# Optimization experiments

Hardware: AMD Instinct MI355X
Metric: run time of the kernel (lower is better)

## Reference

```python
import jax, jax.numpy as jnp
import numpy as np

LOG_STD_MAX = 2.0
LOG_STD_MIN = -5.0
N_LAYERS = 10
HID = 512
OBS = 21
ACT = 8
OVERALL = HID * (N_LAYERS + 1)          # 5632
IN_DIM = OBS + OVERALL                   # 5653
OUT_DIM = OVERALL + ACT                  # 5640
BATCH = 8192


def _block_banded_weight(rng):
    # staircase partitions, exactly as layer_init
    in_d = [0, OBS] + [OBS + HID * i for i in range(1, N_LAYERS + 2)]
    out_d = [0] + [HID * i for i in range(1, N_LAYERS + 2)] + [OUT_DIM]
    W = np.zeros((OUT_DIM, IN_DIM), dtype=np.float32)
    for i in range(N_LAYERS + 2):
        r0, r1 = out_d[i], out_d[i + 1]
        c0, c1 = in_d[i], in_d[i + 1]
        fan_in = c1 - c0
        std = np.sqrt(2.0 / fan_in)  # kaiming_normal_ fan_in, gain sqrt(2)
        W[r0:r1, c0:c1] = rng.standard_normal((r1 - r0, c1 - c0)).astype(np.float32) * std
    return jnp.asarray(W)


def setup_inputs() -> dict:
    key = jax.random.key(0)
    k1, k2, k3, k4, k5, k6 = jax.random.split(key, 6)
    rng = np.random.default_rng(0)
    return {
        "obs": jax.random.normal(k1, (BATCH, OBS), dtype=jnp.float32),
        "hidden0": jax.random.uniform(k2, (BATCH, OVERALL), dtype=jnp.float32),
        "prev_mean": jax.random.normal(k3, (BATCH, ACT), dtype=jnp.float32),
        "prev_logstd": jax.random.normal(k4, (BATCH, ACT), dtype=jnp.float32),
        "W_mean": _block_banded_weight(rng),
        "b_mean": jnp.zeros((OUT_DIM,), dtype=jnp.float32),
        "W_logstd": jax.random.normal(k5, (ACT, IN_DIM), dtype=jnp.float32) / np.sqrt(IN_DIM),
        "b_logstd": jax.random.normal(k6, (ACT,), dtype=jnp.float32) * 0.01,
    }


def reference(obs, hidden0, prev_mean, prev_logstd, W_mean, b_mean, W_logstd, b_logstd):
    x = jnp.concatenate([obs, hidden0], axis=1)            # [B, IN_DIM]
    new_x = x @ W_mean.T + b_mean                          # [B, OUT_DIM]
    new_hidden = jax.nn.relu(new_x[:, :-ACT])              # [B, OVERALL]
    new_mean = new_x[:, -ACT:]                             # [B, ACT]
    new_log_std = x @ W_logstd.T + b_logstd                # [B, ACT]
    # outputs come from the PREVIOUS step's (mean, log_std)
    log_std = jnp.tanh(prev_logstd)
    log_std = LOG_STD_MIN + 0.5 * (LOG_STD_MAX - LOG_STD_MIN) * (log_std + 1.0)
    return (prev_mean, log_std, new_hidden, new_mean, new_log_std)
```

## Files before the change

kernel.cpp:

```cpp
#include <hip/hip_runtime.h>
#include <math.h>

typedef unsigned short u16;
typedef unsigned int u32;
typedef __attribute__((ext_vector_type(8))) short short8;
typedef __attribute__((ext_vector_type(4))) float float4v;

#define BATCH   8192
#define OBS     21
#define HID     512
#define NL      10
#define OVERALL 5632
#define IN_DIM  5653
#define OUT_DIM 5640
#define ACT     8

#define O_PM   0
#define O_LS   65536
#define O_NH   131072
#define O_NM   (131072 + BATCH*OVERALL)
#define O_NLS  (O_NM + 65536)

#define WSP_TOTAL (10*512*512)
#define WSP_BYTES ((size_t)WSP_TOTAL * 2)

__device__ __forceinline__ u16 f2bf(float f) {
    u32 u = __float_as_uint(f);
    u32 r = (u + 0x7fffu + ((u >> 16) & 1u)) >> 16;
    return (u16)r;
}
__device__ __forceinline__ u32 pkbf(float a, float b) {
    return (u32)f2bf(a) | ((u32)f2bf(b) << 16);
}
__device__ __forceinline__ void gload_lds16(const void* g, void* l) {
    __builtin_amdgcn_global_load_lds(
        (const __attribute__((address_space(1))) char*)g,
        (__attribute__((address_space(3))) char*)l, 16, 0, 0);
}

__global__ __launch_bounds__(256) void k_pack(const float* __restrict__ Wm,
                                              u16* __restrict__ ws) {
    int idx = blockIdx.x * 256 + threadIdx.x;
    if (idx >= WSP_TOTAL) return;
    int z = idx >> 18;
    int rem = idx & 262143;
    int n = rem >> 9, k = rem & 511;
    float v = Wm[(size_t)(512 * (z + 1) + n) * IN_DIM + OBS + 512 * z + k];
    ws[idx] = f2bf(v);
}

#define BM 128
#define BN 128
#define BK 32
#define A_LD 40
__global__ __launch_bounds__(256, 2) void k_gemm(const float* __restrict__ X,
                                                 const float* __restrict__ Wm_raw,
                                                 const u16* __restrict__ Wp,
                                                 const float* __restrict__ b_mean,
                                                 float* __restrict__ out_h,
                                                 int packed) {
    __shared__ __attribute__((aligned(16))) u16 As[BM * A_LD];
    __shared__ __attribute__((aligned(16))) u16 Bs[BN * BK];
    int t = threadIdx.x;
    int wave = t >> 6, lane = t & 63;
    int quad = lane >> 4, r16 = lane & 15;
    int gm = blockIdx.x * BM;
    int gn = blockIdx.y * BN;
    int z = blockIdx.z;
    int wm = (wave >> 1) * 64;
    int wn = (wave & 1) * 64;
    int ar = t >> 1;
    int ah = t & 1;

    const float* Arow = X + (size_t)(gm + ar) * OVERALL + z * 512 + ah * 16;

    float4v acc[4][4];
#pragma unroll
    for (int i = 0; i < 4; i++)
#pragma unroll
        for (int j = 0; j < 4; j++) acc[i][j] = (float4v)0.f;

    for (int k0 = 0; k0 < 512; k0 += BK) {
        __syncthreads();
        {
            const float* ga = Arow + k0;
            float4 v0 = *(const float4*)(ga);
            float4 v1 = *(const float4*)(ga + 4);
            float4 v2 = *(const float4*)(ga + 8);
            float4 v3 = *(const float4*)(ga + 12);
            uint4 p0, p1;
            p0.x = pkbf(v0.x, v0.y); p0.y = pkbf(v0.z, v0.w);
            p0.z = pkbf(v1.x, v1.y); p0.w = pkbf(v1.z, v1.w);
            p1.x = pkbf(v2.x, v2.y); p1.y = pkbf(v2.z, v2.w);
            p1.z = pkbf(v3.x, v3.y); p1.w = pkbf(v3.z, v3.w);
            *(uint4*)&As[ar * A_LD + ah * 16] = p0;
            *(uint4*)&As[ar * A_LD + ah * 16 + 8] = p1;
        }
        if (packed) {
#pragma unroll
            for (int it = 0; it < 2; ++it) {
                int n = it * 64 + wave * 16 + (lane >> 2);
                int kk = (lane & 3) * 8;
                const u16* gb = Wp + (size_t)z * (512 * 512) + (size_t)(gn + n) * 512 + k0 + kk;
                gload_lds16(gb, (char*)Bs + it * 4096 + wave * 1024);
            }
        } else {
            int n = t >> 1, h = t & 1;
            const float* gb = Wm_raw + (size_t)(512 * (z + 1) + gn + n) * IN_DIM
                              + OBS + 512 * z + k0 + h * 16;
#pragma unroll
            for (int e = 0; e < 16; e += 2)
                *(u32*)&Bs[n * BK + h * 16 + e] = pkbf(gb[e], gb[e + 1]);
        }
        __syncthreads();

        short8 af[4], bf[4];
#pragma unroll
        for (int i = 0; i < 4; i++) {
            af[i] = *(const short8*)&As[(wm + i * 16 + r16) * A_LD + quad * 8];
            bf[i] = *(const short8*)&Bs[(wn + i * 16 + r16) * BK + quad * 8];
        }
#pragma unroll
        for (int i = 0; i < 4; i++)
#pragma unroll
            for (int j = 0; j < 4; j++)
                acc[i][j] = __builtin_amdgcn_mfma_f32_16x16x32_bf16(af[i], bf[j], acc[i][j], 0, 0, 0);
    }

    int colblock = 512 * (z + 1);
#pragma unroll
    for (int j = 0; j < 4; j++) {
        int n_loc = gn + wn + j * 16 + r16;
        float bias = b_mean[colblock + n_loc];
#pragma unroll
        for (int i = 0; i < 4; i++) {
            int m0 = gm + wm + i * 16 + quad * 4;
#pragma unroll
            for (int r = 0; r < 4; r++) {
                float v = acc[i][j][r] + bias;
                out_h[(size_t)(m0 + r) * OVERALL + colblock + n_loc] = fmaxf(v, 0.f);
            }
        }
    }
}

__global__ __launch_bounds__(256) void k_block0(const float* __restrict__ obs,
                                                const float* __restrict__ Wm,
                                                const float* __restrict__ b_mean,
                                                float* __restrict__ out_h) {
    __shared__ float obs_s[8 * OBS];
    int t = threadIdx.x;
    int b0 = blockIdx.x * 8;
    if (t < 8 * OBS) obs_s[t] = obs[(size_t)b0 * OBS + t];
    __syncthreads();
#pragma unroll
    for (int half = 0; half < 2; ++half) {
        int n = half * 256 + t;
        float w[OBS];
#pragma unroll
        for (int k = 0; k < OBS; k++) w[k] = Wm[(size_t)n * IN_DIM + k];
        float bias = b_mean[n];
#pragma unroll 2
        for (int r = 0; r < 8; r++) {
            float a = bias;
#pragma unroll
            for (int k = 0; k < OBS; k++) a += obs_s[r * OBS + k] * w[k];
            out_h[(size_t)(b0 + r) * OVERALL + n] = fmaxf(a, 0.f);
        }
    }
}

__global__ __launch_bounds__(256) void k_thin(const float* __restrict__ obs,
                                              const float* __restrict__ X,
                                              const float* __restrict__ Wm,
                                              const float* __restrict__ Wls,
                                              const float* __restrict__ b_mean,
                                              const float* __restrict__ b_logstd,
                                              float* __restrict__ out_mean,
                                              float* __restrict__ out_ls) {
    int t = threadIdx.x, wave = t >> 6, lane = t & 63;
    int b0 = (blockIdx.x * 4 + wave) * 4;

    float als[4][8], amn[4][8];
#pragma unroll
    for (int r = 0; r < 4; r++)
#pragma unroll
        for (int n = 0; n < 8; n++) { als[r][n] = 0.f; amn[r][n] = 0.f; }

    for (int j = 0; j < 22; j++) {
        int k = j * 256 + lane * 4;
        float x[4][4];
#pragma unroll
        for (int r = 0; r < 4; r++)
            *(float4*)x[r] = *(const float4*)(X + (size_t)(b0 + r) * OVERALL + k);
#pragma unroll
        for (int n = 0; n < 8; n++) {
            const float* wp = Wls + (size_t)n * IN_DIM + OBS + k;
            float w0 = wp[0], w1 = wp[1], w2 = wp[2], w3 = wp[3];
#pragma unroll
            for (int r = 0; r < 4; r++) {
                als[r][n] += x[r][0] * w0 + x[r][1] * w1 + x[r][2] * w2 + x[r][3] * w3;
            }
        }
        if (j >= 20) {
#pragma unroll
            for (int n = 0; n < 8; n++) {
                const float* wp = Wm + (size_t)(OVERALL + n) * IN_DIM + OBS + k;
                float w0 = wp[0], w1 = wp[1], w2 = wp[2], w3 = wp[3];
#pragma unroll
                for (int r = 0; r < 4; r++) {
                    amn[r][n] += x[r][0] * w0 + x[r][1] * w1 + x[r][2] * w2 + x[r][3] * w3;
                }
            }
        }
    }
    if (lane < OBS) {
#pragma unroll
        for (int r = 0; r < 4; r++) {
            float xo = obs[(size_t)(b0 + r) * OBS + lane];
#pragma unroll
            for (int n = 0; n < 8; n++)
                als[r][n] += xo * Wls[(size_t)n * IN_DIM + lane];
        }
    }
#pragma unroll
    for (int s = 1; s < 64; s <<= 1) {
#pragma unroll
        for (int r = 0; r < 4; r++)
#pragma unroll
            for (int n = 0; n < 8; n++) {
                als[r][n] += __shfl_xor(als[r][n], s, 64);
                amn[r][n] += __shfl_xor(amn[r][n], s, 64);
            }
    }
    if (lane == 0) {
#pragma unroll
        for (int r = 0; r < 4; r++)
#pragma unroll
            for (int n = 0; n < 8; n++) {
                out_ls[(size_t)(b0 + r) * ACT + n] = als[r][n] + b_logstd[n];
                out_mean[(size_t)(b0 + r) * ACT + n] = amn[r][n] + b_mean[OVERALL + n];
            }
    }
}

__global__ __launch_bounds__(256) void k_small(const float* __restrict__ pm,
                                               const float* __restrict__ pls,
                                               float* __restrict__ o0,
                                               float* __restrict__ o1) {
    int i = blockIdx.x * 256 + threadIdx.x;
    float4 a = *(const float4*)(pm + (size_t)i * 4);
    *(float4*)(o0 + (size_t)i * 4) = a;
    float4 b = *(const float4*)(pls + (size_t)i * 4);
    float4 o;
    o.x = -5.f + 3.5f * (tanhf(b.x) + 1.f);
    o.y = -5.f + 3.5f * (tanhf(b.y) + 1.f);
    o.z = -5.f + 3.5f * (tanhf(b.z) + 1.f);
    o.w = -5.f + 3.5f * (tanhf(b.w) + 1.f);
    *(float4*)(o1 + (size_t)i * 4) = o;
}

extern "C" void kernel_launch(void* const* d_in, const int* in_sizes, int n_in,
                              void* d_out, int out_size, void* d_ws, size_t ws_size,
                              hipStream_t stream) {
    const float* obs         = (const float*)d_in[0];
    const float* hidden0     = (const float*)d_in[1];
    const float* prev_mean   = (const float*)d_in[2];
    const float* prev_logstd = (const float*)d_in[3];
    const float* W_mean      = (const float*)d_in[4];
    const float* b_mean      = (const float*)d_in[5];
    const float* W_logstd    = (const float*)d_in[6];
    const float* b_logstd    = (const float*)d_in[7];

    float* out   = (float*)d_out;
    float* o_pm  = out + O_PM;
    float* o_ls  = out + O_LS;
    float* o_nh  = out + O_NH;
    float* o_nm  = out + O_NM;
    float* o_nls = out + O_NLS;
    u16*   ws    = (u16*)d_ws;

    int packed = (ws != nullptr && ws_size >= WSP_BYTES) ? 1 : 0;

    if (packed) {
        k_pack<<<(WSP_TOTAL + 255) / 256, 256, 0, stream>>>(W_mean, ws);
    }
    k_gemm<<<dim3(BATCH / BM, 512 / BN, NL), 256, 0, stream>>>(
        hidden0, W_mean, ws, b_mean, o_nh, packed);
    k_block0<<<BATCH / 8, 256, 0, stream>>>(obs, W_mean, b_mean, o_nh);
    k_thin<<<BATCH / 16, 256, 0, stream>>>(obs, hidden0, W_mean, W_logstd,
                                           b_mean, b_logstd, o_nm, o_nls);
    k_small<<<64, 256, 0, stream>>>(prev_mean, prev_logstd, o_pm, o_ls);
}
```

Baseline: 512.5 us.

## Fuse thin logstd/mean projections into block GEMM with full-width N tiles

Replaces the separate thin fp32 reduction kernel by computing the logstd and final-mean projections with bf16 MFMA inside the block-diagonal GEMM, each block reusing the activation tile already staged in LDS. Logstd partials are accumulated across z-slices with atomics into a pre-zeroed buffer. The GEMM now uses 1024-thread blocks covering all 512 output columns, with a swizzled B layout in LDS and register prefetch of the next A tile, so each activation tile is read once per slice instead of four times. The obs-block kernel caches its weights in LDS, and the small elementwise work merges into a finish kernel. The trade-offs are atomics, bf16 rounding on the logstd path, and a large LDS footprint per block.

Measured after the change: 452.3 us. 1.13x faster.

```diff
diff --git a/kernel.cpp b/kernel.cpp
--- a/kernel.cpp
+++ b/kernel.cpp
@@ -12,7 +12,6 @@
 #define NL      10
 #define OVERALL 5632
 #define IN_DIM  5653
-#define OUT_DIM 5640
 #define ACT     8
 
 #define O_PM   0
@@ -50,214 +49,242 @@
 }
 
 #define BM 128
-#define BN 128
 #define BK 32
-#define A_LD 40
-__global__ __launch_bounds__(256, 2) void k_gemm(const float* __restrict__ X,
-                                                 const float* __restrict__ Wm_raw,
-                                                 const u16* __restrict__ Wp,
-                                                 const float* __restrict__ b_mean,
-                                                 float* __restrict__ out_h,
-                                                 int packed) {
-    __shared__ __attribute__((aligned(16))) u16 As[BM * A_LD];
-    __shared__ __attribute__((aligned(16))) u16 Bs[BN * BK];
+#define LDA 40
+__global__ __launch_bounds__(1024, 4) void k_fused(
+        const float* __restrict__ X,
+        const float* __restrict__ Wm_raw,
+        const u16* __restrict__ Wp,
+        const float* __restrict__ Wls_raw,
+        const float* __restrict__ b_mean,
+        float* __restrict__ out_h,
+        float* __restrict__ out_ls,
+        float* __restrict__ out_mean,
+        int packed) {
+    __shared__ __attribute__((aligned(16))) u16 As[BM * LDA];
+    __shared__ __attribute__((aligned(16))) u16 Bs[512 * 32];
+    __shared__ __attribute__((aligned(16))) u16 Wt[16 * 520];
+    u16* Wt2 = (u16*)Bs;
+
     int t = threadIdx.x;
-    int wave = t >> 6, lane = t & 63;
+    int w = t >> 6, lane = t & 63;
     int quad = lane >> 4, r16 = lane & 15;
     int gm = blockIdx.x * BM;
-    int gn = blockIdx.y * BN;
-    int z = blockIdx.z;
-    int wm = (wave >> 1) * 64;
-    int wn = (wave & 1) * 64;
-    int ar = t >> 1;
-    int ah = t & 1;
-
-    const float* Arow = X + (size_t)(gm + ar) * OVERALL + z * 512 + ah * 16;
+    int z = blockIdx.y;
+    bool mainz = (z < 10);
+    int wm = (w >> 3) * 64;
+    int wn = (w & 7) * 64;
+
+    {
+        int n = t >> 7;
+        int k4 = (t & 127) * 4;
+        const float* wr = Wls_raw + (size_t)n * IN_DIM + OBS + z * 512 + k4;
+        u16* dst = &Wt[n * 520 + k4];
+        dst[0] = f2bf(wr[0]); dst[1] = f2bf(wr[1]);
+        dst[2] = f2bf(wr[2]); dst[3] = f2bf(wr[3]);
+        if (!mainz) {
+            const float* wr2 = Wm_raw + (size_t)(OVERALL + n) * IN_DIM + OBS + z * 512 + k4;
+            u16* d2 = &Wt2[n * 520 + k4];
+            d2[0] = f2bf(wr2[0]); d2[1] = f2bf(wr2[1]);
+            d2[2] = f2bf(wr2[2]); d2[3] = f2bf(wr2[3]);
+        }
+    }
+
+    int arow = t >> 3;
+    int acol = (t & 7) * 4;
+    const float* gA = X + (size_t)(gm + arow) * OVERALL + (size_t)z * 512 + acol;
+    float4 areg = *(const float4*)(gA);
 
     float4v acc[4][4];
 #pragma unroll
     for (int i = 0; i < 4; i++)
 #pragma unroll
         for (int j = 0; j < 4; j++) acc[i][j] = (float4v)0.f;
-
-    for (int k0 = 0; k0 < 512; k0 += BK) {
+    float4v accL = (float4v)0.f;
+
+    for (int it = 0; it < 16; ++it) {
+        int k0 = it * BK;
         __syncthreads();
         {
-            const float* ga = Arow + k0;
-            float4 v0 = *(const float4*)(ga);
-            float4 v1 = *(const float4*)(ga + 4);
-            float4 v2 = *(const float4*)(ga + 8);
-            float4 v3 = *(const float4*)(ga + 12);
-            uint4 p0, p1;
-            p0.x = pkbf(v0.x, v0.y); p0.y = pkbf(v0.z, v0.w);
-            p0.z = pkbf(v1.x, v1.y); p0.w = pkbf(v1.z, v1.w);
-            p1.x = pkbf(v2.x, v2.y); p1.y = pkbf(v2.z, v2.w);
-            p1.z = pkbf(v3.x, v3.y); p1.w = pkbf(v3.z, v3.w);
-            *(uint4*)&As[ar * A_LD + ah * 16] = p0;
-            *(uint4*)&As[ar * A_LD + ah * 16 + 8] = p1;
-        }
-        if (packed) {
-#pragma unroll
-            for (int it = 0; it < 2; ++it) {
-                int n = it * 64 + wave * 16 + (lane >> 2);
-                int kk = (lane & 3) * 8;
-                const u16* gb = Wp + (size_t)z * (512 * 512) + (size_t)(gn + n) * 512 + k0 + kk;
-                gload_lds16(gb, (char*)Bs + it * 4096 + wave * 1024);
-            }
-        } else {
-            int n = t >> 1, h = t & 1;
-            const float* gb = Wm_raw + (size_t)(512 * (z + 1) + gn + n) * IN_DIM
-                              + OBS + 512 * z + k0 + h * 16;
-#pragma unroll
-            for (int e = 0; e < 16; e += 2)
-                *(u32*)&Bs[n * BK + h * 16 + e] = pkbf(gb[e], gb[e + 1]);
+            uint2 p;
+            p.x = pkbf(areg.x, areg.y);
+            p.y = pkbf(areg.z, areg.w);
+            *(uint2*)&As[arow * LDA + acol] = p;
+        }
+        if (mainz) {
+            if (packed) {
+#pragma unroll
+                for (int i2 = 0; i2 < 2; ++i2) {
+                    int base_row = i2 * 256 + w * 16;
+                    int row = base_row + (lane >> 2);
+                    int slot = lane & 3;
+                    int j = (slot - row) & 3;
+                    const u16* g = Wp + (size_t)z * 262144 + (size_t)row * 512 + k0 + j * 8;
+                    gload_lds16(g, (char*)Bs + base_row * 64);
+                }
+            } else {
+#pragma unroll
+                for (int i2 = 0; i2 < 2; ++i2) {
+                    int row = i2 * 256 + w * 16 + (lane >> 2);
+                    int slot = lane & 3;
+                    int j = (slot - row) & 3;
+                    const float* g = Wm_raw + (size_t)(512 * (z + 1) + row) * IN_DIM
+                                     + OBS + (size_t)z * 512 + k0 + j * 8;
+                    uint4 q;
+                    q.x = pkbf(g[0], g[1]); q.y = pkbf(g[2], g[3]);
+                    q.z = pkbf(g[4], g[5]); q.w = pkbf(g[6], g[7]);
+                    *(uint4*)&Bs[row * 32 + slot * 8] = q;
+                }
+            }
         }
         __syncthreads();
-
-        short8 af[4], bf[4];
-#pragma unroll
-        for (int i = 0; i < 4; i++) {
-            af[i] = *(const short8*)&As[(wm + i * 16 + r16) * A_LD + quad * 8];
-            bf[i] = *(const short8*)&Bs[(wn + i * 16 + r16) * BK + quad * 8];
-        }
-#pragma unroll
-        for (int i = 0; i < 4; i++)
-#pragma unroll
-            for (int j = 0; j < 4; j++)
-                acc[i][j] = __builtin_amdgcn_mfma_f32_16x16x32_bf16(af[i], bf[j], acc[i][j], 0, 0, 0);
-    }
-
-    int colblock = 512 * (z + 1);
-#pragma unroll
-    for (int j = 0; j < 4; j++) {
-        int n_loc = gn + wn + j * 16 + r16;
-        float bias = b_mean[colblock + n_loc];
-#pragma unroll
-        for (int i = 0; i < 4; i++) {
-            int m0 = gm + wm + i * 16 + quad * 4;
+        if (it < 15) areg = *(const float4*)(gA + (it + 1) * BK);
+
+        if (mainz) {
+            short8 bfr[4];
+#pragma unroll
+            for (int j = 0; j < 4; j++) {
+                int n = wn + j * 16 + r16;
+                int s = (quad + n) & 3;
+                bfr[j] = *(const short8*)&Bs[n * 32 + s * 8];
+            }
+#pragma unroll
+            for (int i2 = 0; i2 < 4; i2++) {
+                short8 af = *(const short8*)&As[(wm + i2 * 16 + r16) * LDA + quad * 8];
+#pragma unroll
+                for (int j = 0; j < 4; j++)
+                    acc[i2][j] = __builtin_amdgcn_mfma_f32_16x16x32_bf16(af, bfr[j], acc[i2][j], 0, 0, 0);
+            }
+        }
+        if (w < 8) {
+            short8 aL = *(const short8*)&As[(w * 16 + r16) * LDA + quad * 8];
+            short8 bL = *(const short8*)&Wt[r16 * 520 + k0 + quad * 8];
+            accL = __builtin_amdgcn_mfma_f32_16x16x32_bf16(aL, bL, accL, 0, 0, 0);
+        } else if (!mainz) {
+            short8 aL = *(const short8*)&As[((w - 8) * 16 + r16) * LDA + quad * 8];
+            short8 bL = *(const short8*)&Wt2[r16 * 520 + k0 + quad * 8];
+            accL = __builtin_amdgcn_mfma_f32_16x16x32_bf16(aL, bL, accL, 0, 0, 0);
+        }
+    }
+
+    if (mainz) {
+        int colblock = (z + 1) * 512;
+#pragma unroll
+        for (int j = 0; j < 4; j++) {
+            int n_loc = wn + j * 16 + r16;
+            float bias = b_mean[colblock + n_loc];
+#pragma unroll
+            for (int i2 = 0; i2 < 4; i2++) {
+                int m0 = gm + wm + i2 * 16 + quad * 4;
+#pragma unroll
+                for (int r = 0; r < 4; r++) {
+                    float v = acc[i2][j][r] + bias;
+                    out_h[(size_t)(m0 + r) * OVERALL + colblock + n_loc] = fmaxf(v, 0.f);
+                }
+            }
+        }
+    }
+    if (w < 8) {
+        if (r16 < ACT) {
 #pragma unroll
             for (int r = 0; r < 4; r++) {
-                float v = acc[i][j][r] + bias;
-                out_h[(size_t)(m0 + r) * OVERALL + colblock + n_loc] = fmaxf(v, 0.f);
-            }
-        }
-    }
-}
-
+                int row = gm + w * 16 + quad * 4 + r;
+                atomicAdd(&out_ls[(size_t)row * ACT + r16], accL[r]);
+            }
+        }
+    } else if (!mainz) {
+        if (r16 < ACT) {
+            float bias = b_mean[OVERALL + r16];
+#pragma unroll
+            for (int r = 0; r < 4; r++) {
+                int row = gm + (w - 8) * 16 + quad * 4 + r;
+                out_mean[(size_t)row * ACT + r16] = accL[r] + bias;
+            }
+        }
+    }
+}
+
+#define B0_ROWS 32
 __global__ __launch_bounds__(256) void k_block0(const float* __restrict__ obs,
                                                 const float* __restrict__ Wm,
                                                 const float* __restrict__ b_mean,
                                                 float* __restrict__ out_h) {
-    __shared__ float obs_s[8 * OBS];
+    __shared__ float w0[OBS * 512];
+    __shared__ float bias_s[512];
+    __shared__ float obs_s[B0_ROWS * OBS];
     int t = threadIdx.x;
-    int b0 = blockIdx.x * 8;
-    if (t < 8 * OBS) obs_s[t] = obs[(size_t)b0 * OBS + t];
+    int b0 = blockIdx.x * B0_ROWS;
+    for (int i = t; i < OBS * 512; i += 256) {
+        int n = i / OBS, k = i - n * OBS;
+        w0[k * 512 + n] = Wm[(size_t)n * IN_DIM + k];
+    }
+    for (int i = t; i < 512; i += 256) bias_s[i] = b_mean[i];
+    for (int i = t; i < B0_ROWS * OBS; i += 256) obs_s[i] = obs[(size_t)b0 * OBS + i];
     __syncthreads();
-#pragma unroll
-    for (int half = 0; half < 2; ++half) {
-        int n = half * 256 + t;
-        float w[OBS];
-#pragma unroll
-        for (int k = 0; k < OBS; k++) w[k] = Wm[(size_t)n * IN_DIM + k];
-        float bias = b_mean[n];
-#pragma unroll 2
-        for (int r = 0; r < 8; r++) {
-            float a = bias;
-#pragma unroll
-            for (int k = 0; k < OBS; k++) a += obs_s[r * OBS + k] * w[k];
-            out_h[(size_t)(b0 + r) * OVERALL + n] = fmaxf(a, 0.f);
-        }
-    }
-}
-
-__global__ __launch_bounds__(256) void k_thin(const float* __restrict__ obs,
-                                              const float* __restrict__ X,
-                                              const float* __restrict__ Wm,
-                                              const float* __restrict__ Wls,
-                                              const float* __restrict__ b_mean,
-                                              const float* __restrict__ b_logstd,
-                                              float* __restrict__ out_mean,
-                                              float* __restrict__ out_ls) {
-    int t = threadIdx.x, wave = t >> 6, lane = t & 63;
-    int b0 = (blockIdx.x * 4 + wave) * 4;
-
-    float als[4][8], amn[4][8];
-#pragma unroll
-    for (int r = 0; r < 4; r++)
-#pragma unroll
-        for (int n = 0; n < 8; n++) { als[r][n] = 0.f; amn[r][n] = 0.f; }
-
-    for (int j = 0; j < 22; j++) {
-        int k = j * 256 + lane * 4;
-        float x[4][4];
-#pragma unroll
-        for (int r = 0; r < 4; r++)
-            *(float4*)x[r] = *(const float4*)(X + (size_t)(b0 + r) * OVERALL + k);
-#pragma unroll
-        for (int n = 0; n < 8; n++) {
-            const float* wp = Wls + (size_t)n * IN_DIM + OBS + k;
-            float w0 = wp[0], w1 = wp[1], w2 = wp[2], w3 = wp[3];
-#pragma unroll
-            for (int r = 0; r < 4; r++) {
-                als[r][n] += x[r][0] * w0 + x[r][1] * w1 + x[r][2] * w2 + x[r][3] * w3;
-            }
-        }
-        if (j >= 20) {
-#pragma unroll
-            for (int n = 0; n < 8; n++) {
-                const float* wp = Wm + (size_t)(OVERALL + n) * IN_DIM + OBS + k;
-                float w0 = wp[0], w1 = wp[1], w2 = wp[2], w3 = wp[3];
-#pragma unroll
-                for (int r = 0; r < 4; r++) {
-                    amn[r][n] += x[r][0] * w0 + x[r][1] * w1 + x[r][2] * w2 + x[r][3] * w3;
-                }
-            }
-        }
-    }
-    if (lane < OBS) {
-#pragma unroll
-        for (int r = 0; r < 4; r++) {
-            float xo = obs[(size_t)(b0 + r) * OBS + lane];
-#pragma unroll
-            for (int n = 0; n < 8; n++)
-                als[r][n] += xo * Wls[(size_t)n * IN_DIM + lane];
-        }
-    }
-#pragma unroll
-    for (int s = 1; s < 64; s <<= 1) {
-#pragma unroll
-        for (int r = 0; r < 4; r++)
-#pragma unroll
-            for (int n = 0; n < 8; n++) {
-                als[r][n] += __shfl_xor(als[r][n], s, 64);
-                amn[r][n] += __shfl_xor(amn[r][n], s, 64);
-            }
-    }
-    if (lane == 0) {
-#pragma unroll
-        for (int r = 0; r < 4; r++)
-#pragma unroll
-            for (int n = 0; n < 8; n++) {
-                out_ls[(size_t)(b0 + r) * ACT + n] = als[r][n] + b_logstd[n];
-                out_mean[(size_t)(b0 + r) * ACT + n] = amn[r][n] + b_mean[OVERALL + n];
-            }
-    }
-}
-
-__global__ __launch_bounds__(256) void k_small(const float* __restrict__ pm,
-                                               const float* __restrict__ pls,
-                                               float* __restrict__ o0,
-                                               float* __restrict__ o1) {
-    int i = blockIdx.x * 256 + threadIdx.x;
-    float4 a = *(const float4*)(pm + (size_t)i * 4);
-    *(float4*)(o0 + (size_t)i * 4) = a;
-    float4 b = *(const float4*)(pls + (size_t)i * 4);
-    float4 o;
-    o.x = -5.f + 3.5f * (tanhf(b.x) + 1.f);
-    o.y = -5.f + 3.5f * (tanhf(b.y) + 1.f);
-    o.z = -5.f + 3.5f * (tanhf(b.z) + 1.f);
-    o.w = -5.f + 3.5f * (tanhf(b.w) + 1.f);
-    *(float4*)(o1 + (size_t)i * 4) = o;
+
+    int n0 = (t & 127) * 4;
+    int rh = t >> 7;
+#pragma unroll 4
+    for (int r = 0; r < 16; r++) {
+        int row = rh * 16 + r;
+        float acc0 = bias_s[n0], acc1 = bias_s[n0 + 1];
+        float acc2 = bias_s[n0 + 2], acc3 = bias_s[n0 + 3];
+#pragma unroll
+        for (int k = 0; k < OBS; k++) {
+            float xo = obs_s[row * OBS + k];
+            const float* wr = &w0[k * 512 + n0];
+            acc0 += xo * wr[0]; acc1 += xo * wr[1];
+            acc2 += xo * wr[2]; acc3 += xo * wr[3];
+        }
+        float4 o;
+        o.x = fmaxf(acc0, 0.f); o.y = fmaxf(acc1, 0.f);
+        o.z = fmaxf(acc2, 0.f); o.w = fmaxf(acc3, 0.f);
+        *(float4*)&out_h[(size_t)(b0 + row) * OVERALL + n0] = o;
+    }
+}
+
+__global__ __launch_bounds__(256) void k_finish(const float* __restrict__ obs,
+                                                const float* __restrict__ Wls,
+                                                const float* __restrict__ b_logstd,
+                                                const float* __restrict__ pm,
+                                                const float* __restrict__ pls,
+                                                float* __restrict__ o_pm,
+                                                float* __restrict__ o_lstd,
+                                                float* __restrict__ o_nls) {
+    __shared__ float wobs[ACT * OBS];
+    __shared__ float bls[ACT];
+    int t = threadIdx.x;
+    if (t < ACT * OBS) wobs[t] = Wls[(size_t)(t / OBS) * IN_DIM + (t % OBS)];
+    if (t < ACT) bls[t] = b_logstd[t];
+    __syncthreads();
+    int row = blockIdx.x * 256 + t;
+    float ob[OBS];
+#pragma unroll
+    for (int k = 0; k < OBS; k++) ob[k] = obs[(size_t)row * OBS + k];
+#pragma unroll
+    for (int n = 0; n < ACT; n++) {
+        float a = bls[n];
+#pragma unroll
+        for (int k = 0; k < OBS; k++) a += ob[k] * wobs[n * OBS + k];
+        o_nls[(size_t)row * ACT + n] += a;
+    }
+    float4 p0 = *(const float4*)(pm + (size_t)row * ACT);
+    float4 p1 = *(const float4*)(pm + (size_t)row * ACT + 4);
+    *(float4*)(o_pm + (size_t)row * ACT) = p0;
+    *(float4*)(o_pm + (size_t)row * ACT + 4) = p1;
+    float4 l0 = *(const float4*)(pls + (size_t)row * ACT);
+    float4 l1 = *(const float4*)(pls + (size_t)row * ACT + 4);
+    float4 q0, q1;
+    q0.x = -5.f + 3.5f * (tanhf(l0.x) + 1.f);
+    q0.y = -5.f + 3.5f * (tanhf(l0.y) + 1.f);
+    q0.z = -5.f + 3.5f * (tanhf(l0.z) + 1.f);
+    q0.w = -5.f + 3.5f * (tanhf(l0.w) + 1.f);
+    q1.x = -5.f + 3.5f * (tanhf(l1.x) + 1.f);
+    q1.y = -5.f + 3.5f * (tanhf(l1.y) + 1.f);
+    q1.z = -5.f + 3.5f * (tanhf(l1.z) + 1.f);
+    q1.w = -5.f + 3.5f * (tanhf(l1.w) + 1.f);
+    *(float4*)(o_lstd + (size_t)row * ACT) = q0;
+    *(float4*)(o_lstd + (size_t)row * ACT + 4) = q1;
 }
 
 extern "C" void kernel_launch(void* const* d_in, const int* in_sizes, int n_in,
@@ -285,10 +312,11 @@
     if (packed) {
         k_pack<<<(WSP_TOTAL + 255) / 256, 256, 0, stream>>>(W_mean, ws);
     }
-    k_gemm<<<dim3(BATCH / BM, 512 / BN, NL), 256, 0, stream>>>(
-        hidden0, W_mean, ws, b_mean, o_nh, packed);
-    k_block0<<<BATCH / 8, 256, 0, stream>>>(obs, W_mean, b_mean, o_nh);
-    k_thin<<<BATCH / 16, 256, 0, stream>>>(obs, hidden0, W_mean, W_logstd,
-                                           b_mean, b_logstd, o_nm, o_nls);
-    k_small<<<64, 256, 0, stream>>>(prev_mean, prev_logstd, o_pm, o_ls);
-}
+    hipMemsetAsync(o_nls, 0, (size_t)BATCH * ACT * sizeof(float), stream);
+    k_fused<<<dim3(BATCH / BM, NL + 1), 1024, 0, stream>>>(
+        hidden0, W_mean, ws, W_logstd, b_mean, o_nh, o_nls, o_nm, packed);
+    k_block0<<<BATCH / B0_ROWS, 256, 0, stream>>>(obs, W_mean, b_mean, o_nh);
+    k_finish<<<BATCH / 256, 256, 0, stream>>>(obs, W_logstd, b_logstd,
+                                              prev_mean, prev_logstd,
+                                              o_pm, o_ls, o_nls);
+}
```
